# Kernel optimization log

Measured on AMD Instinct MI355X. Metric: run time of the kernel, lower is better.

## Reference

```python
import jax, jax.numpy as jnp
import numpy as np

L = 512          # profile HMM model length (number of match states)
S = 25           # alphabet size (input_dim)
BATCH = 128
T_LEN = 1024
TINY = np.finfo(np.float32).tiny


def setup_inputs():
    key = jax.random.key(0)
    ks = jax.random.split(key, 18)
    def n(k, shape):
        return 0.1 * jax.random.normal(k, shape, dtype=jnp.float32)
    return {
        "seq": jax.random.randint(ks[0], (BATCH, T_LEN), 0, S),
        "em_kernel": n(ks[1], (L, S)),
        "ins_kernel": n(ks[2], (S,)),
        "flank_kernel": n(ks[3], (1,)),
        "btm": n(ks[4], (L,)),
        "m2e": n(ks[5], (L,)),
        "mtm": n(ks[6], (L - 1,)),
        "m2i": n(ks[7], (L - 1,)),
        "i2m": n(ks[8], (L - 1,)),
        "i2i": n(ks[9], (L - 1,)),
        "mtd": n(ks[10], (L,)),
        "dtm": n(ks[11], (L,)),
        "dtd": n(ks[12], (L - 1,)),
        "lf_loop": n(ks[13], (1,)),
        "lf_exit": n(ks[14], (1,)),
        "e2u": n(ks[15], (1,)),
        "e2r": n(ks[16], (1,)),
        "e2t": n(ks[17], (1,)),
    }


def _build_hmm(em_kernel, ins_kernel, flank_kernel, btm, m2e, mtm, m2i, i2m, i2i,
               mtd, dtm, dtd, lf_loop, lf_exit, e2u, e2r, e2t):
    """Build implicit transition matrix A [q,q], emission matrix B [q,S+1], init dist [q].
    Explicit states begin/end/delete are marginalized out (silent states), yielding the
    implicit transition structure of the profile HMM (match skips via delete chains)."""
    Lm = em_kernel.shape[0]
    q = 2 * Lm + 3                      # LF, M_1..M_L, I_1..I_{L-1}, U, RF, T
    U, RF, TM = 2 * Lm, 2 * Lm + 1, 2 * Lm + 2
    idx = jnp.arange(Lm)
    dt = em_kernel.dtype
    # per-source-state softmax over explicit outgoing edges
    begin_p = jax.nn.softmax(jnp.concatenate([btm, mtd[:1]]))            # begin -> M_j / D_1
    btm_p = begin_p[:Lm]
    mp = jax.nn.softmax(jnp.stack([mtm, m2i, m2e[:Lm - 1], mtd[1:]], axis=-1), axis=-1)
    mtm_p, m2i_p, m2e_p, mtd_mid = mp[:, 0], mp[:, 1], mp[:, 2], mp[:, 3]
    ip = jax.nn.softmax(jnp.stack([i2m, i2i], axis=-1), axis=-1)
    i2m_p, i2i_p = ip[:, 0], ip[:, 1]
    dp = jax.nn.softmax(jnp.stack([dtm[:Lm - 1], dtd], axis=-1), axis=-1)
    dtm_p = jnp.concatenate([dp[:, 0], jnp.ones((1,), dt)])              # D_L -> end with prob 1
    dtd_p = dp[:, 1]
    fp = jax.nn.softmax(jnp.concatenate([lf_loop, lf_exit]))            # shared flank kernels
    floop, fexit = fp[0], fp[1]
    ep = jax.nn.softmax(jnp.concatenate([e2u, e2r, e2t]))               # end -> U / RF / T
    # marginalize silent delete chain. Sk[i,k]: P(src_i => target via deletes),
    # src_0 = begin, src_i = M_i; target M_{k+2} for k<=L-2, end for k=L-1.
    mtd_p = jnp.concatenate([begin_p[Lm:], mtd_mid])                    # begin->D_1, M_i->D_{i+1}
    cp_log = jnp.concatenate([jnp.zeros((1,), dt), jnp.cumsum(jnp.log(dtd_p))])
    Sk = mtd_p[:, None] * jnp.exp(cp_log[None, :] - cp_log[:, None]) * dtm_p[None, :]
    Sk = jnp.where(idx[None, :] >= idx[:, None], Sk, jnp.zeros((), dt))
    enter = btm_p + jnp.pad(Sk[0, :Lm - 1], (1, 0))                      # begin => M_j
    begin_end = Sk[0, Lm - 1]                                            # begin => end (all deleted)
    m2e_tot = jnp.concatenate([m2e_p + Sk[1:, Lm - 1], jnp.ones((1,), dt)])
    A = jnp.zeros((q, q), dt)
    Mblk = jnp.zeros((Lm, Lm), dt).at[idx[:-1], idx[1:]].set(mtm_p)
    Mblk = Mblk.at[0:Lm - 1, 1:Lm].add(Sk[1:Lm, 0:Lm - 1])               # match skips (j>=i+2)
    A = A.at[1:Lm + 1, 1:Lm + 1].set(Mblk)
    A = A.at[0, 0].set(floop)
    A = A.at[0, 1:Lm + 1].set(fexit * enter)
    A = A.at[0, U].set(fexit * begin_end * ep[0])
    A = A.at[0, RF].set(fexit * begin_end * ep[1])
    A = A.at[0, TM].set(fexit * begin_end * ep[2])
    A = A.at[jnp.arange(1, Lm), jnp.arange(Lm + 1, 2 * Lm)].set(m2i_p)   # M_i -> I_i
    A = A.at[1:Lm + 1, U].set(m2e_tot * ep[0])
    A = A.at[1:Lm + 1, RF].set(m2e_tot * ep[1])
    A = A.at[1:Lm + 1, TM].set(m2e_tot * ep[2])
    A = A.at[jnp.arange(Lm + 1, 2 * Lm), jnp.arange(2, Lm + 1)].set(i2m_p)  # I_i -> M_{i+1}
    A = A.at[jnp.arange(Lm + 1, 2 * Lm), jnp.arange(Lm + 1, 2 * Lm)].set(i2i_p)
    A = A.at[U, 1:Lm + 1].set(fexit * enter)
    A = A.at[U, U].set(floop + fexit * begin_end * ep[0])
    A = A.at[U, RF].set(fexit * begin_end * ep[1])
    A = A.at[U, TM].set(fexit * begin_end * ep[2])
    A = A.at[RF, RF].set(floop)
    A = A.at[RF, TM].set(fexit)
    A = A.at[TM, TM].set(1.0)
    # emission matrix per make_default_emission_matrix: [ins; em; ins x (L+1)] rows,
    # softmax, zero pad column, terminal one-hot row -> [2L+3, S+1]
    rows = jnp.concatenate([ins_kernel[None], em_kernel,
                            jnp.tile(ins_kernel[None], (Lm + 1, 1))], axis=0)
    Bm = jax.nn.softmax(rows, axis=-1)
    Bm = jnp.concatenate([Bm, jnp.zeros((2 * Lm + 2, 1), dt)], axis=-1)
    s_alph = em_kernel.shape[1]
    Bm = jnp.concatenate([Bm, jax.nn.one_hot(jnp.array([s_alph]), s_alph + 1, dtype=dt)], axis=0)
    # initial distribution: start in left flank w.p. sigmoid(flank_init), else enter model
    p0 = jax.nn.sigmoid(flank_kernel[0])
    init = jnp.zeros((q,), dt).at[0].set(p0)
    init = init.at[1:Lm + 1].set((1 - p0) * enter)
    init = init.at[U].set((1 - p0) * begin_end * ep[0])
    init = init.at[RF].set((1 - p0) * begin_end * ep[1])
    init = init.at[TM].set((1 - p0) * begin_end * ep[2])
    return A, Bm, init


def _forward(seq, *params):
    A, Bm, init = _build_hmm(*params)
    # emission probs per timestep: matvec(B, one_hot(x)) == column gather
    E = Bm.T[seq]                        # [batch, T, q]
    alpha = init[None, :] * E[:, 0]
    s = alpha.sum(-1, keepdims=True) + TINY
    ll = jnp.log(s[:, 0])
    alpha = alpha / s

    def step(carry, Et):
        a, l = carry
        a = Et * (a @ A)                 # forward-algorithm recurrence + scaling
        sn = a.sum(-1, keepdims=True) + TINY
        return (a / sn, l + jnp.log(sn[:, 0])), None

    (alpha, ll), _ = jax.lax.scan(step, (alpha, ll), jnp.swapaxes(E[:, 1:], 0, 1))
    return ll                            # [batch] sequence log-likelihoods


def reference(seq, em_kernel, ins_kernel, flank_kernel, btm, m2e, mtm, m2i, i2m, i2i,
              mtd, dtm, dtd, lf_loop, lf_exit, e2u, e2r, e2t):
    return _forward(seq, em_kernel, ins_kernel, flank_kernel, btm, m2e, mtm, m2i, i2m,
                    i2i, mtd, dtm, dtd, lf_loop, lf_exit, e2u, e2r, e2t)
```

## Files before the change

### kernel.cpp

```cpp
#include <hip/hip_runtime.h>
#include <math.h>

#define LM 512
#define TLEN 1024
#define TINY_F 1.17549435e-38f

#define OFF_ENTER 0
#define OFF_MTM   512
#define OFF_I2M   1024
#define OFF_DTM   1536
#define OFF_WC    2048
#define OFF_MC    2560
#define OFF_M2I   3072
#define OFF_I2I   3584
#define OFF_M2E   4096
#define OFF_INS   4608
#define OFF_SC    4640
#define OFF_EMB   5120

typedef float v2f __attribute__((ext_vector_type(2)));

__device__ __forceinline__ v2f pfma(v2f a, v2f b, v2f c) {
    return __builtin_elementwise_fma(a, b, c);
}
__device__ __forceinline__ v2f vs(float c) { return (v2f){c, c}; }

template<int Ctrl, int RowMask>
__device__ __forceinline__ float fdpp(float oldv, float src) {
    int r = __builtin_amdgcn_update_dpp(
        __builtin_bit_cast(int, oldv), __builtin_bit_cast(int, src),
        Ctrl, RowMask, 0xF, false);
    return __builtin_bit_cast(float, r);
}

__device__ __forceinline__ float rdlane63(float v) {
    return __builtin_bit_cast(float,
        __builtin_amdgcn_readlane(__builtin_bit_cast(int, v), 63));
}

__device__ __forceinline__ float wave_sum_to63(float v) {
    v += fdpp<0x111, 0xF>(0.f, v);
    v += fdpp<0x112, 0xF>(0.f, v);
    v += fdpp<0x114, 0xF>(0.f, v);
    v += fdpp<0x118, 0xF>(0.f, v);
    v += fdpp<0x142, 0xA>(0.f, v);
    v += fdpp<0x143, 0xC>(0.f, v);
    return v;
}

__global__ __launch_bounds__(512) void hmm_setup(
    const float* __restrict__ em, const float* __restrict__ ins,
    const float* __restrict__ flank, const float* __restrict__ btm,
    const float* __restrict__ m2e, const float* __restrict__ mtm,
    const float* __restrict__ m2i, const float* __restrict__ i2m,
    const float* __restrict__ i2i, const float* __restrict__ mtd,
    const float* __restrict__ dtm, const float* __restrict__ dtd,
    const float* __restrict__ lfl, const float* __restrict__ lfe,
    const float* __restrict__ e2u, const float* __restrict__ e2r,
    const float* __restrict__ e2t, float* __restrict__ P)
{
    __shared__ float beginp[513];
    __shared__ float mtdp[512], dtmp[512], dtdp[512], cplog[512];
    __shared__ float mtmp[512], m2ip[512], m2ep[512], i2mp[512], i2ip[512];
    __shared__ float rbuf[512], rbuf2[512];
    const int j = threadIdx.x;

    float eb = expf(btm[j]);
    rbuf[j] = eb;
    __syncthreads();
    for (int s = 256; s > 0; s >>= 1) {
        if (j < s) rbuf[j] += rbuf[j + s];
        __syncthreads();
    }
    float e512 = expf(mtd[0]);
    float tot = rbuf[0] + e512;
    beginp[j] = eb / tot;
    if (j == 0) { beginp[512] = e512 / tot; mtdp[0] = e512 / tot; }

    if (j < 511) {
        float a = expf(mtm[j]), b = expf(m2i[j]), c = expf(m2e[j]), d = expf(mtd[j + 1]);
        float s = a + b + c + d;
        mtmp[j] = a / s; m2ip[j] = b / s; m2ep[j] = c / s; mtdp[j + 1] = d / s;
        float ia = expf(i2m[j]), ib = expf(i2i[j]); s = ia + ib;
        i2mp[j] = ia / s; i2ip[j] = ib / s;
        float da = expf(dtm[j]), db = expf(dtd[j]); s = da + db;
        dtmp[j] = da / s; dtdp[j] = db / s;
    }
    if (j == 511) dtmp[511] = 1.0f;
    __syncthreads();

    {
        float lw = (j >= 1) ? logf(dtdp[j - 1]) : 0.f;
        rbuf[j] = lw;
        __syncthreads();
        float* bufs[2] = { rbuf, rbuf2 };
        int cur = 0;
        for (int off = 1; off < 512; off <<= 1) {
            float v = bufs[cur][j];
            if (j >= off) v += bufs[cur][j - off];
            bufs[cur ^ 1][j] = v;
            cur ^= 1;
            __syncthreads();
        }
        cplog[j] = bufs[cur][j];
    }
    __syncthreads();

    if (j == 0) {
        float sm = 0.f;
        for (int s = 0; s < 25; ++s) sm += expf(ins[s]);
        for (int s = 0; s < 25; ++s) P[OFF_INS + s] = expf(ins[s]) / sm;
        float fl = expf(lfl[0]), fe = expf(lfe[0]); float fs = fl + fe;
        float floop = fl / fs, fexit = fe / fs;
        float eu = expf(e2u[0]), er = expf(e2r[0]), et = expf(e2t[0]);
        float es = eu + er + et; float ep0 = eu / es, ep1 = er / es;
        float p0 = 1.0f / (1.0f + expf(-flank[0]));
        float be = mtdp[0] * expf(cplog[511]) * dtmp[511];
        P[OFF_SC + 0] = floop;
        P[OFF_SC + 1] = fexit;
        P[OFF_SC + 2] = p0;
        P[OFF_SC + 3] = fexit * be * ep0;
        P[OFF_SC + 4] = fexit * be * ep1;
        P[OFF_SC + 5] = ep0;
        P[OFF_SC + 6] = ep1;
        P[OFF_SC + 7] = (1.0f - p0) * be * ep0;
        P[OFF_SC + 8] = (1.0f - p0) * be * ep1;
        P[OFF_SC + 9] = 1.0f - p0;
    }
    __syncthreads();

    float en = beginp[j];
    if (j >= 1) en += mtdp[0] * expf(cplog[j - 1]) * dtmp[j - 1];
    P[OFF_ENTER + j] = en;
    P[OFF_MTM + j] = (j >= 1) ? mtmp[j - 1] : 0.f;
    P[OFF_I2M + j] = (j >= 1) ? i2mp[j - 1] : 0.f;
    P[OFF_DTM + j] = (j >= 1) ? dtmp[j - 1] : 0.f;
    P[OFF_WC  + j] = (j >= 1) ? mtdp[j]     : 0.f;
    P[OFF_MC  + j] = (j >= 1) ? dtdp[j - 1] : 0.f;
    P[OFF_M2I + j] = (j < 511) ? m2ip[j] : 0.f;
    P[OFF_I2I + j] = (j < 511) ? i2ip[j] : 0.f;
    P[OFF_M2E + j] = (j < 511)
        ? (m2ep[j] + mtdp[j + 1] * expf(cplog[511] - cplog[j + 1]))
        : 1.0f;

    {
        const float* row = em + j * 25;
        float mx = row[0];
        for (int s = 1; s < 25; ++s) mx = fmaxf(mx, row[s]);
        float sm = 0.f;
        for (int s = 0; s < 25; ++s) sm += expf(row[s] - mx);
        float inv = 1.0f / sm;
        int lanej = j >> 3, e = j & 7;
        int pos = ((e >> 2) << 8) | (lanej << 2) | (e & 3);
        for (int s = 0; s < 25; ++s)
            P[OFF_EMB + s * 512 + pos] = expf(row[s] - mx) * inv;
    }
}

__global__ __launch_bounds__(64, 1) void hmm_forward(
    const int* __restrict__ seq, const float* __restrict__ P,
    float* __restrict__ out)
{
    __shared__ __align__(16) float sEmb[25 * 512];
    __shared__ float sIns[32];
    __shared__ __align__(16) int sSeq[TLEN + 4];

    const int lane = threadIdx.x;
    const int b = blockIdx.x;
    const int base = lane * 8;

    {
        const float4* src = (const float4*)(P + OFF_EMB);
        float4* dst = (float4*)sEmb;
#pragma unroll 5
        for (int k = lane; k < 25 * 128; k += 64) dst[k] = src[k];
        if (lane < 32) sIns[lane] = P[OFF_INS + (lane < 25 ? lane : 0)];
        const int4* s4 = (const int4*)(seq + b * TLEN);
        int4* d4 = (int4*)sSeq;
#pragma unroll
        for (int k = lane; k < 256; k += 64) d4[k] = s4[k];
        if (lane < 4) sSeq[TLEN + lane] = 0;
    }

    float mtm_[8], i2m_[8], dtm_[8], wC_[8], mC_[8];
    v2f enter2[4], m2i2[4], i2i2[4], m2e2[4], dtmM2[4];
    {
        float enter_[8], m2i_[8], i2i_[8], m2e_[8], dtmM_[8];
#pragma unroll
        for (int e = 0; e < 8; ++e) {
            enter_[e] = P[OFF_ENTER + base + e];
            mtm_[e]   = P[OFF_MTM + base + e];
            i2m_[e]   = P[OFF_I2M + base + e];
            dtm_[e]   = P[OFF_DTM + base + e];
            wC_[e]    = P[OFF_WC + base + e];
            mC_[e]    = P[OFF_MC + base + e];
            m2i_[e]   = P[OFF_M2I + base + e];
            i2i_[e]   = P[OFF_I2I + base + e];
            m2e_[e]   = P[OFF_M2E + base + e];
        }
        float Mp = mC_[0];
        dtmM_[0] = dtm_[0];
#pragma unroll
        for (int e = 1; e < 8; ++e) { dtmM_[e] = dtm_[e] * Mp; Mp *= mC_[e]; }
#pragma unroll
        for (int p = 0; p < 4; ++p) {
            enter2[p] = (v2f){enter_[2*p], enter_[2*p+1]};
            m2i2[p]   = (v2f){m2i_[2*p],   m2i_[2*p+1]};
            i2i2[p]   = (v2f){i2i_[2*p],   i2i_[2*p+1]};
            m2e2[p]   = (v2f){m2e_[2*p],   m2e_[2*p+1]};
            dtmM2[p]  = (v2f){dtmM_[2*p],  dtmM_[2*p+1]};
        }
    }
    const float floop = P[OFF_SC + 0], fexit = P[OFF_SC + 1], p0 = P[OFF_SC + 2];
    const float ep0 = P[OFF_SC + 5], ep1 = P[OFF_SC + 6];
    const float omp0 = P[OFF_SC + 9];

    __syncthreads();

    v2f am2[4], ai2[4];
#define AM(e) ((e) & 1 ? am2[(e) >> 1].y : am2[(e) >> 1].x)
#define AI(e) ((e) & 1 ? ai2[(e) >> 1].y : ai2[(e) >> 1].x)

    v2f EmA2[4], EmB2[4];
    float EiA, EiB;
    {
        int s0 = sSeq[0];
        const float4* c4 = (const float4*)(sEmb + (s0 << 9) + (lane << 2));
        float4 xx = c4[0], yy = c4[64];
        EmA2[0] = (v2f){xx.x, xx.y}; EmA2[1] = (v2f){xx.z, xx.w};
        EmA2[2] = (v2f){yy.x, yy.y}; EmA2[3] = (v2f){yy.z, yy.w};
        EiA = sIns[s0];
    }
#pragma unroll
    for (int p = 0; p < 4; ++p) {
        am2[p] = EmA2[p] * vs(omp0) * enter2[p];
        ai2[p] = (v2f){0.f, 0.f};
    }
    float f0 = p0 * EiA;
    float U  = 0.f;
    float RF = 0.f;
    float ll2 = 0.f;

    int symN = sSeq[1];
    {
        const float4* c4 = (const float4*)(sEmb + (symN << 9) + (lane << 2));
        float4 xx = c4[0], yy = c4[64];
        EmA2[0] = (v2f){xx.x, xx.y}; EmA2[1] = (v2f){xx.z, xx.w};
        EmA2[2] = (v2f){yy.x, yy.y}; EmA2[3] = (v2f){yy.z, yy.w};
        EiA = sIns[symN];
    }
    symN = sSeq[2];
    int sidx = 3;

#define STEP(EmC2, EiC, EmN2, EiN, DO_NORM)                                    \
  {                                                                            \
    {        \
      const float4* c4 = (const float4*)(sEmb + (symN << 9) + (lane << 2));    \
      float4 xx = c4[0], yy = c4[64];                                          \
      EmN2[0] = (v2f){xx.x, xx.y}; EmN2[1] = (v2f){xx.z, xx.w};                \
      EmN2[2] = (v2f){yy.x, yy.y}; EmN2[3] = (v2f){yy.z, yy.w};                \
      EiN = sIns[symN];                                                        \
      symN = sSeq[sidx]; ++sidx;                                               \
    }                                                                          \
    float amL = fdpp<0x138, 0xF>(0.f, am2[3].y);                               \
    float aiL = fdpp<0x138, 0xF>(0.f, ai2[3].y);                               \
                 \
    float Apre[8];                                                             \
    Apre[0] = amL * wC_[0];                                                    \
    _Pragma("unroll")                                                          \
    for (int e = 1; e < 8; ++e)                                                \
      Apre[e] = fmaf(Apre[e - 1], mC_[e], AM(e - 1) * wC_[e]);                 \
         \
    float carry = fdpp<0x138, 0xF>(0.f, Apre[7]);                              \
                \
    v2f dv = am2[0] * m2e2[0];                                                 \
    dv = pfma(am2[1], m2e2[1], dv);                                            \
    dv = pfma(am2[2], m2e2[2], dv);                                            \
    dv = pfma(am2[3], m2e2[3], dv);                                            \
    float dsum = rdlane63(wave_sum_to63(dv.x + dv.y));                         \
                          \
    float aFU = (f0 + U) * fexit;                                              \
    float nf0 = EiC * (f0 * floop);                                            \
    float nU  = EiC * fmaf(dsum, ep0, U * floop);                              \
    float nRF = EiC * fmaf(dsum, ep1, RF * floop);                             \
    f0 = nf0; U = nU; RF = nRF;                                                \
     \
    v2f tp[4];                                                                 \
    tp[0].x = fmaf(amL, mtm_[0], aiL * i2m_[0]);                               \
    tp[0].y = fmaf(AM(0), mtm_[1], AI(0) * i2m_[1]);                           \
    tp[1].x = fmaf(AM(1), mtm_[2], AI(1) * i2m_[2]);                           \
    tp[1].y = fmaf(AM(2), mtm_[3], AI(2) * i2m_[3]);                           \
    tp[2].x = fmaf(AM(3), mtm_[4], AI(3) * i2m_[4]);                           \
    tp[2].y = fmaf(AM(4), mtm_[5], AI(4) * i2m_[5]);                           \
    tp[3].x = fmaf(AM(5), mtm_[6], AI(5) * i2m_[6]);                           \
    tp[3].y = fmaf(AM(6), mtm_[7], AI(6) * i2m_[7]);                           \
                                  \
    v2f EiC2 = vs(EiC);                                                        \
    ai2[0] = EiC2 * pfma(am2[0], m2i2[0], ai2[0] * i2i2[0]);                   \
    ai2[1] = EiC2 * pfma(am2[1], m2i2[1], ai2[1] * i2i2[1]);                   \
    ai2[2] = EiC2 * pfma(am2[2], m2i2[2], ai2[2] * i2i2[2]);                   \
    ai2[3] = EiC2 * pfma(am2[3], m2i2[3], ai2[3] * i2i2[3]);                   \
      \
    v2f aFU2 = vs(aFU), carry2 = vs(carry);                                    \
    tp[0] = pfma(aFU2, enter2[0], tp[0]);                                      \
    tp[1] = pfma(aFU2, enter2[1], tp[1]);                                      \
    tp[2] = pfma(aFU2, enter2[2], tp[2]);                                      \
    tp[3] = pfma(aFU2, enter2[3], tp[3]);                                      \
    tp[0].y = fmaf(dtm_[1], Apre[0], tp[0].y);                                 \
    tp[1].x = fmaf(dtm_[2], Apre[1], tp[1].x);                                 \
    tp[1].y = fmaf(dtm_[3], Apre[2], tp[1].y);                                 \
    tp[2].x = fmaf(dtm_[4], Apre[3], tp[2].x);                                 \
    tp[2].y = fmaf(dtm_[5], Apre[4], tp[2].y);                                 \
    tp[3].x = fmaf(dtm_[6], Apre[5], tp[3].x);                                 \
    tp[3].y = fmaf(dtm_[7], Apre[6], tp[3].y);                                 \
    tp[0] = pfma(dtmM2[0], carry2, tp[0]);                                     \
    tp[1] = pfma(dtmM2[1], carry2, tp[1]);                                     \
    tp[2] = pfma(dtmM2[2], carry2, tp[2]);                                     \
    tp[3] = pfma(dtmM2[3], carry2, tp[3]);                                     \
    am2[0] = EmC2[0] * tp[0];                                                  \
    am2[1] = EmC2[1] * tp[1];                                                  \
    am2[2] = EmC2[2] * tp[2];                                                  \
    am2[3] = EmC2[3] * tp[3];                                                  \
       \
    if (DO_NORM) {                                                             \
      v2f ns = am2[0] + ai2[0];                                                \
      ns += am2[1] + ai2[1];                                                   \
      ns += am2[2] + ai2[2];                                                   \
      ns += am2[3] + ai2[3];                                                   \
      float sl = ns.x + ns.y + ((lane == 0) ? (f0 + U + RF) : 0.f);            \
      float s = rdlane63(wave_sum_to63(sl)) + TINY_F;                          \
      ll2 += __log2f(s);                                                       \
      float inv = 1.0f / s;                                                    \
      v2f inv2 = vs(inv);                                                      \
      am2[0] *= inv2; am2[1] *= inv2; am2[2] *= inv2; am2[3] *= inv2;          \
      ai2[0] *= inv2; ai2[1] *= inv2; ai2[2] *= inv2; ai2[3] *= inv2;          \
      f0 *= inv; U *= inv; RF *= inv;                                          \
    }                                                                          \
  }

#define PAIR(NORM2)                                                            \
    STEP(EmA2, EiA, EmB2, EiB, 0)                                              \
    STEP(EmB2, EiB, EmA2, EiA, NORM2)

    for (int c = 0; c < 63; ++c) {
        PAIR(0) PAIR(0) PAIR(0) PAIR(0)
        PAIR(0) PAIR(0) PAIR(0) PAIR(1)
    }
    for (int p = 0; p < 7; ++p) {
        PAIR(0)
    }
    STEP(EmA2, EiA, EmB2, EiB, 1)
#undef PAIR
#undef STEP
#undef AM
#undef AI

    if (lane == 0) out[b] = ll2 * 0.69314718055994530942f;
}

extern "C" void kernel_launch(void* const* d_in, const int* in_sizes, int n_in,
                              void* d_out, int out_size, void* d_ws, size_t ws_size,
                              hipStream_t stream) {
    const int*   seq   = (const int*)d_in[0];
    const float* em    = (const float*)d_in[1];
    const float* ins   = (const float*)d_in[2];
    const float* flank = (const float*)d_in[3];
    const float* btm   = (const float*)d_in[4];
    const float* m2e   = (const float*)d_in[5];
    const float* mtm   = (const float*)d_in[6];
    const float* m2i   = (const float*)d_in[7];
    const float* i2m   = (const float*)d_in[8];
    const float* i2i   = (const float*)d_in[9];
    const float* mtd   = (const float*)d_in[10];
    const float* dtm   = (const float*)d_in[11];
    const float* dtd   = (const float*)d_in[12];
    const float* lfl   = (const float*)d_in[13];
    const float* lfe   = (const float*)d_in[14];
    const float* e2u   = (const float*)d_in[15];
    const float* e2r   = (const float*)d_in[16];
    const float* e2t   = (const float*)d_in[17];
    float* P = (float*)d_ws;
    float* out = (float*)d_out;

    hipLaunchKernelGGL(hmm_setup, dim3(1), dim3(512), 0, stream,
        em, ins, flank, btm, m2e, mtm, m2i, i2m, i2i, mtd, dtm, dtd,
        lfl, lfe, e2u, e2r, e2t, P);
    hipLaunchKernelGGL(hmm_forward, dim3(128), dim3(64), 0, stream, seq, P, out);
}
```

Measured before the change: 291.6 us.

## Factor insert emission out of recurrence and normalize less often

Match emissions are divided by the insert-state emission probability of the same symbol. This makes every state share a per-timestep factor, which is pulled out of the recurrence and added to the log-likelihood once as a wave-reduced sum of log2 insert probabilities. The per-step multiplies by the insert emission on the insert, flank, U and RF states are removed. Rescaling now happens every 64 steps instead of every 16, which cuts wave reductions but raises the risk of float overflow or underflow in the unscaled alpha.

```diff
diff --git a/kernel.cpp b/kernel.cpp
--- a/kernel.cpp
+++ b/kernel.cpp
@@ -63,7 +63,15 @@
     __shared__ float mtdp[512], dtmp[512], dtdp[512], cplog[512];
     __shared__ float mtmp[512], m2ip[512], m2ep[512], i2mp[512], i2ip[512];
     __shared__ float rbuf[512], rbuf2[512];
+    __shared__ float inspS[25];
     const int j = threadIdx.x;
+
+    if (j < 25) {
+        float sm = 0.f;
+        for (int s = 0; s < 25; ++s) sm += expf(ins[s]);
+        inspS[j] = expf(ins[j]) / sm;
+        P[OFF_INS + j] = log2f(inspS[j]);
+    }
 
     float eb = expf(btm[j]);
     rbuf[j] = eb;
@@ -107,24 +115,16 @@
     __syncthreads();
 
     if (j == 0) {
-        float sm = 0.f;
-        for (int s = 0; s < 25; ++s) sm += expf(ins[s]);
-        for (int s = 0; s < 25; ++s) P[OFF_INS + s] = expf(ins[s]) / sm;
         float fl = expf(lfl[0]), fe = expf(lfe[0]); float fs = fl + fe;
         float floop = fl / fs, fexit = fe / fs;
         float eu = expf(e2u[0]), er = expf(e2r[0]), et = expf(e2t[0]);
         float es = eu + er + et; float ep0 = eu / es, ep1 = er / es;
         float p0 = 1.0f / (1.0f + expf(-flank[0]));
-        float be = mtdp[0] * expf(cplog[511]) * dtmp[511];
         P[OFF_SC + 0] = floop;
         P[OFF_SC + 1] = fexit;
         P[OFF_SC + 2] = p0;
-        P[OFF_SC + 3] = fexit * be * ep0;
-        P[OFF_SC + 4] = fexit * be * ep1;
         P[OFF_SC + 5] = ep0;
         P[OFF_SC + 6] = ep1;
-        P[OFF_SC + 7] = (1.0f - p0) * be * ep0;
-        P[OFF_SC + 8] = (1.0f - p0) * be * ep1;
         P[OFF_SC + 9] = 1.0f - p0;
     }
     __syncthreads();
@@ -153,7 +153,7 @@
         int lanej = j >> 3, e = j & 7;
         int pos = ((e >> 2) << 8) | (lanej << 2) | (e & 3);
         for (int s = 0; s < 25; ++s)
-            P[OFF_EMB + s * 512 + pos] = expf(row[s] - mx) * inv;
+            P[OFF_EMB + s * 512 + pos] = (expf(row[s] - mx) * inv) / inspS[s];
     }
 }
 
@@ -162,7 +162,7 @@
     float* __restrict__ out)
 {
     __shared__ __align__(16) float sEmb[25 * 512];
-    __shared__ float sIns[32];
+    __shared__ float sLogEi[32];
     __shared__ __align__(16) int sSeq[TLEN + 4];
 
     const int lane = threadIdx.x;
@@ -174,12 +174,21 @@
         float4* dst = (float4*)sEmb;
 #pragma unroll 5
         for (int k = lane; k < 25 * 128; k += 64) dst[k] = src[k];
-        if (lane < 32) sIns[lane] = P[OFF_INS + (lane < 25 ? lane : 0)];
+        if (lane < 32) sLogEi[lane] = P[OFF_INS + (lane < 25 ? lane : 0)];
         const int4* s4 = (const int4*)(seq + b * TLEN);
         int4* d4 = (int4*)sSeq;
 #pragma unroll
         for (int k = lane; k < 256; k += 64) d4[k] = s4[k];
         if (lane < 4) sSeq[TLEN + lane] = 0;
+    }
+    __syncthreads();
+
+    float llE;
+    {
+        float le = 0.f;
+#pragma unroll
+        for (int k = 0; k < 16; ++k) le += sLogEi[sSeq[lane * 16 + k]];
+        llE = rdlane63(wave_sum_to63(le));
     }
 
     float mtm_[8], i2m_[8], dtm_[8], wC_[8], mC_[8];
@@ -215,31 +224,27 @@
     const float ep0 = P[OFF_SC + 5], ep1 = P[OFF_SC + 6];
     const float omp0 = P[OFF_SC + 9];
 
-    __syncthreads();
-
     v2f am2[4], ai2[4];
 #define AM(e) ((e) & 1 ? am2[(e) >> 1].y : am2[(e) >> 1].x)
 #define AI(e) ((e) & 1 ? ai2[(e) >> 1].y : ai2[(e) >> 1].x)
 
     v2f EmA2[4], EmB2[4];
-    float EiA, EiB;
     {
         int s0 = sSeq[0];
         const float4* c4 = (const float4*)(sEmb + (s0 << 9) + (lane << 2));
         float4 xx = c4[0], yy = c4[64];
         EmA2[0] = (v2f){xx.x, xx.y}; EmA2[1] = (v2f){xx.z, xx.w};
         EmA2[2] = (v2f){yy.x, yy.y}; EmA2[3] = (v2f){yy.z, yy.w};
-        EiA = sIns[s0];
     }
 #pragma unroll
     for (int p = 0; p < 4; ++p) {
         am2[p] = EmA2[p] * vs(omp0) * enter2[p];
         ai2[p] = (v2f){0.f, 0.f};
     }
-    float f0 = p0 * EiA;
+    float f0 = p0;
     float U  = 0.f;
     float RF = 0.f;
-    float ll2 = 0.f;
+    float ll2 = llE;
 
     int symN = sSeq[1];
     {
@@ -247,19 +252,17 @@
         float4 xx = c4[0], yy = c4[64];
         EmA2[0] = (v2f){xx.x, xx.y}; EmA2[1] = (v2f){xx.z, xx.w};
         EmA2[2] = (v2f){yy.x, yy.y}; EmA2[3] = (v2f){yy.z, yy.w};
-        EiA = sIns[symN];
     }
     symN = sSeq[2];
     int sidx = 3;
 
-#define STEP(EmC2, EiC, EmN2, EiN, DO_NORM)                                    \
+#define STEP(EmC2, EmN2, DO_NORM)                                              \
   {                                                                            \
-    {        \
+    {                \
       const float4* c4 = (const float4*)(sEmb + (symN << 9) + (lane << 2));    \
       float4 xx = c4[0], yy = c4[64];                                          \
       EmN2[0] = (v2f){xx.x, xx.y}; EmN2[1] = (v2f){xx.z, xx.w};                \
       EmN2[2] = (v2f){yy.x, yy.y}; EmN2[3] = (v2f){yy.z, yy.w};                \
-      EiN = sIns[symN];                                                        \
       symN = sSeq[sidx]; ++sidx;                                               \
     }                                                                          \
     float amL = fdpp<0x138, 0xF>(0.f, am2[3].y);                               \
@@ -278,12 +281,11 @@
     dv = pfma(am2[2], m2e2[2], dv);                                            \
     dv = pfma(am2[3], m2e2[3], dv);                                            \
     float dsum = rdlane63(wave_sum_to63(dv.x + dv.y));                         \
-                          \
+                     \
     float aFU = (f0 + U) * fexit;                                              \
-    float nf0 = EiC * (f0 * floop);                                            \
-    float nU  = EiC * fmaf(dsum, ep0, U * floop);                              \
-    float nRF = EiC * fmaf(dsum, ep1, RF * floop);                             \
-    f0 = nf0; U = nU; RF = nRF;                                                \
+    f0 = f0 * floop;                                                           \
+    U  = fmaf(dsum, ep0, U * floop);                                           \
+    RF = fmaf(dsum, ep1, RF * floop);                                          \
      \
     v2f tp[4];                                                                 \
     tp[0].x = fmaf(amL, mtm_[0], aiL * i2m_[0]);                               \
@@ -294,12 +296,11 @@
     tp[2].y = fmaf(AM(4), mtm_[5], AI(4) * i2m_[5]);                           \
     tp[3].x = fmaf(AM(5), mtm_[6], AI(5) * i2m_[6]);                           \
     tp[3].y = fmaf(AM(6), mtm_[7], AI(6) * i2m_[7]);                           \
-                                  \
-    v2f EiC2 = vs(EiC);                                                        \
-    ai2[0] = EiC2 * pfma(am2[0], m2i2[0], ai2[0] * i2i2[0]);                   \
-    ai2[1] = EiC2 * pfma(am2[1], m2i2[1], ai2[1] * i2i2[1]);                   \
-    ai2[2] = EiC2 * pfma(am2[2], m2i2[2], ai2[2] * i2i2[2]);                   \
-    ai2[3] = EiC2 * pfma(am2[3], m2i2[3], ai2[3] * i2i2[3]);                   \
+      \
+    ai2[0] = pfma(am2[0], m2i2[0], ai2[0] * i2i2[0]);                          \
+    ai2[1] = pfma(am2[1], m2i2[1], ai2[1] * i2i2[1]);                          \
+    ai2[2] = pfma(am2[2], m2i2[2], ai2[2] * i2i2[2]);                          \
+    ai2[3] = pfma(am2[3], m2i2[3], ai2[3] * i2i2[3]);                          \
       \
     v2f aFU2 = vs(aFU), carry2 = vs(carry);                                    \
     tp[0] = pfma(aFU2, enter2[0], tp[0]);                                      \
@@ -339,17 +340,18 @@
   }
 
 #define PAIR(NORM2)                                                            \
-    STEP(EmA2, EiA, EmB2, EiB, 0)                                              \
-    STEP(EmB2, EiB, EmA2, EiA, NORM2)
+    STEP(EmA2, EmB2, 0)                                                        \
+    STEP(EmB2, EmA2, NORM2)
 
     for (int c = 0; c < 63; ++c) {
+        int nf = ((c & 3) == 3);
         PAIR(0) PAIR(0) PAIR(0) PAIR(0)
-        PAIR(0) PAIR(0) PAIR(0) PAIR(1)
+        PAIR(0) PAIR(0) PAIR(0) PAIR(nf)
     }
     for (int p = 0; p < 7; ++p) {
         PAIR(0)
     }
-    STEP(EmA2, EiA, EmB2, EiB, 1)
+    STEP(EmA2, EmB2, 1)
 #undef PAIR
 #undef STEP
 #undef AM
```

Result: faster. 270.4 us (-7.3%).
